# Optimization experiments

Hardware: AMD Instinct MI355X
Metric: run time of the kernel (lower is better)

## Reference

```python
import jax, jax.numpy as jnp
import numpy as np

N_NODES = 50000
N_EDGES = 400000
IN_DIM = 512
OUT_DIM = 512


def setup_inputs() -> dict:
    key = jax.random.key(0)
    k1, k2, k3, k4 = jax.random.split(key, 4)
    x = jax.random.normal(k1, (N_NODES, IN_DIM), dtype=jnp.float32)
    edge_index = jax.random.randint(k2, (2, N_EDGES), 0, N_NODES, dtype=jnp.int64)
    # nn.Linear(in_dim, out_dim): weight [out, in], bias [out]
    W = jax.random.normal(k3, (OUT_DIM, IN_DIM), dtype=jnp.float32) / np.sqrt(IN_DIM)
    b = jax.random.normal(k4, (OUT_DIM,), dtype=jnp.float32) * 0.01
    return {"x": x, "edge_index": edge_index, "W": W, "b": b}


def reference(x, edge_index, W, b):
    n = x.shape[0]
    loops = jnp.arange(n, dtype=edge_index.dtype)
    row = jnp.concatenate([edge_index[0], loops])  # src
    col = jnp.concatenate([edge_index[1], loops])  # dst
    # degree from row counts (matches torch.bincount(row)); self-loops ensure deg >= 1
    deg = jax.ops.segment_sum(jnp.ones(row.shape[0], dtype=x.dtype), row, num_segments=n)
    dis = jax.lax.rsqrt(deg)  # deg^-0.5
    norm = dis[row] * dis[col]  # [E+N]
    h = x @ W.T + b  # [N, out_dim]
    # out[dst] += norm * h[src], fused gather-scale-scatter
    out = jax.ops.segment_sum(norm[:, None] * h[row], col, num_segments=n)
    return jax.nn.relu(out)
```

## Files before the change

### kernel.cpp

```cpp
#include <hip/hip_runtime.h>
#include <hip/hip_bf16.h>

#define K_DIM 512
#define N_DIM 512

typedef __attribute__((ext_vector_type(8))) short s8v;
typedef __attribute__((ext_vector_type(4))) short s4v;
typedef __attribute__((ext_vector_type(4))) float f4v;

__device__ __forceinline__ short f2bf(float f) {
  union { float f; unsigned u; } v; v.f = f;
  unsigned r = (v.u + 0x7FFFu + ((v.u >> 16) & 1u)) >> 16;
  return (short)r;
}
__device__ __forceinline__ float bflo(unsigned u) {
  union { unsigned u; float f; } v; v.u = u << 16; return v.f;
}
__device__ __forceinline__ float bfhi(unsigned u) {
  union { unsigned u; float f; } v; v.u = u & 0xffff0000u; return v.f;
}

__device__ __forceinline__ void gload16(const void* g, void* l) {
  __builtin_amdgcn_global_load_lds(
      (const __attribute__((address_space(1))) void*)g,
      (__attribute__((address_space(3))) void*)l, 16, 0, 0);
}

__device__ __forceinline__ int edge_stride(const int* __restrict__ e32, int lane) {
  int chk = e32[2 * lane + 1];
  unsigned long long m = __ballot(chk == 0);
  return (m == ~0ULL) ? 2 : 1;
}

__global__ __launch_bounds__(256) void k_pre1(const float* __restrict__ W,
    short* __restrict__ Wb, const int* __restrict__ e32, int* __restrict__ outdeg,
    int* __restrict__ indeg, int E, int nbw) {
  int b = blockIdx.x;
  int t = threadIdx.x;
  if (b < nbw) {
    int i = (b * 256 + t) * 4;
    float4 f = *(const float4*)(W + i);
    s4v s; s[0] = f2bf(f.x); s[1] = f2bf(f.y); s[2] = f2bf(f.z); s[3] = f2bf(f.w);
    *(s4v*)(Wb + i) = s;
  } else {
    int st = edge_stride(e32, t & 63);
    int i = (b - nbw) * 256 + t;
    if (i < E) {
      int r = e32[(size_t)i * st];
      int c = e32[(size_t)(E + i) * st];
      atomicAdd(&outdeg[r], 1);
      atomicAdd(&indeg[c], 1);
    }
  }
}

__global__ __launch_bounds__(256) void k_pre2(const int* __restrict__ outdeg,
    float* __restrict__ dis, const int* __restrict__ indeg, int* __restrict__ part,
    int n, int nbd) {
  int b = blockIdx.x;
  if (b < nbd) {
    int i = b * 256 + threadIdx.x;
    if (i < n) dis[i] = rsqrtf((float)(outdeg[i] + 1));
  } else {
    __shared__ int sm[256];
    int lb = b - nbd;
    int i = lb * 256 + threadIdx.x;
    sm[threadIdx.x] = (i < n) ? indeg[i] : 0;
    __syncthreads();
    for (int off = 128; off > 0; off >>= 1) {
      if (threadIdx.x < off) sm[threadIdx.x] += sm[threadIdx.x + off];
      __syncthreads();
    }
    if (threadIdx.x == 0) part[lb] = sm[0];
  }
}

__global__ __launch_bounds__(256) void k_scan(const int* __restrict__ indeg,
    const int* __restrict__ part, int* __restrict__ row_start,
    int* __restrict__ cursor, int n, int nb) {
  __shared__ int sp[256];
  __shared__ int sm[256];
  int t = threadIdx.x, b = blockIdx.x;
  sp[t] = (t < nb) ? part[t] : 0;
  __syncthreads();
  for (int off = 1; off < 256; off <<= 1) {
    int a = (t >= off) ? sp[t - off] : 0;
    __syncthreads();
    sp[t] += a;
    __syncthreads();
  }
  int pOff = (b > 0) ? sp[b - 1] : 0;
  if (b == 0 && t == 255) row_start[n] = sp[255];
  int i = b * 256 + t;
  int v = (i < n) ? indeg[i] : 0;
  sm[t] = v;
  __syncthreads();
  for (int off = 1; off < 256; off <<= 1) {
    int a = (t >= off) ? sm[t - off] : 0;
    __syncthreads();
    sm[t] += a;
    __syncthreads();
  }
  if (i < n) {
    int excl = pOff + sm[t] - v;
    row_start[i] = excl;
    cursor[i] = excl;
  }
}

__global__ __launch_bounds__(256) void k_fillconv(const int* __restrict__ e32,
    int* __restrict__ cursor, int* __restrict__ csr, int E,
    const float* __restrict__ x, const float* __restrict__ dis,
    short* __restrict__ xs, long long totalx, int nbh) {
  int b = blockIdx.x;
  int t = threadIdx.x;
  if (b < nbh) {
    int st = edge_stride(e32, t & 63);
    int i = b * 256 + t;
    if (i < E) {
      int r = e32[(size_t)i * st];
      int c = e32[(size_t)(E + i) * st];
      int p = atomicAdd(&cursor[c], 1);
      csr[p] = r;
    }
  } else {
    long long i = ((long long)(b - nbh) * 256 + t) * 8;
    if (i < totalx) {
      float dv = dis[i >> 9];
      float4 f0 = *(const float4*)(x + i);
      float4 f1 = *(const float4*)(x + i + 4);
      s8v v;
      v[0] = f2bf(dv * f0.x); v[1] = f2bf(dv * f0.y);
      v[2] = f2bf(dv * f0.z); v[3] = f2bf(dv * f0.w);
      v[4] = f2bf(dv * f1.x); v[5] = f2bf(dv * f1.y);
      v[6] = f2bf(dv * f1.z); v[7] = f2bf(dv * f1.w);
      *(s8v*)(xs + i) = v;
    }
  }
}

__device__ __forceinline__ void add8(float* acc, uint4 rv) {
  acc[0] += bflo(rv.x); acc[1] += bfhi(rv.x);
  acc[2] += bflo(rv.y); acc[3] += bfhi(rv.y);
  acc[4] += bflo(rv.z); acc[5] += bfhi(rv.z);
  acc[6] += bflo(rv.w); acc[7] += bfhi(rv.w);
}

__global__ __launch_bounds__(256) void k_agg(const short* __restrict__ xs,
    const float* __restrict__ dis, const int* __restrict__ row_start,
    const int* __restrict__ csr, short* __restrict__ xa, float* __restrict__ s,
    int n) {
  int wid = blockIdx.x * 4 + (threadIdx.x >> 6);
  int nw = gridDim.x * 4;
  int lane = threadIdx.x & 63;
  const short* hl = xs + lane * 8;
  for (int v = wid; v < n; v += nw) {
    float acc[8];
    float accs = 0.f;
    {
      uint4 r = *(const uint4*)(hl + (size_t)v * N_DIM);
      acc[0] = bflo(r.x); acc[1] = bfhi(r.x);
      acc[2] = bflo(r.y); acc[3] = bfhi(r.y);
      acc[4] = bflo(r.z); acc[5] = bfhi(r.z);
      acc[6] = bflo(r.w); acc[7] = bfhi(r.w);
    }
    int sb = __builtin_amdgcn_readfirstlane(row_start[v]);
    int eb = __builtin_amdgcn_readfirstlane(row_start[v + 1]);
    int idx = sb;
    for (; idx + 8 <= eb; idx += 8) {
      int s0 = csr[idx],     s1 = csr[idx + 1], s2 = csr[idx + 2], s3 = csr[idx + 3];
      int s4 = csr[idx + 4], s5 = csr[idx + 5], s6 = csr[idx + 6], s7 = csr[idx + 7];
      uint4 r0 = *(const uint4*)(hl + (size_t)s0 * N_DIM);
      uint4 r1 = *(const uint4*)(hl + (size_t)s1 * N_DIM);
      uint4 r2 = *(const uint4*)(hl + (size_t)s2 * N_DIM);
      uint4 r3 = *(const uint4*)(hl + (size_t)s3 * N_DIM);
      uint4 r4 = *(const uint4*)(hl + (size_t)s4 * N_DIM);
      uint4 r5 = *(const uint4*)(hl + (size_t)s5 * N_DIM);
      uint4 r6 = *(const uint4*)(hl + (size_t)s6 * N_DIM);
      uint4 r7 = *(const uint4*)(hl + (size_t)s7 * N_DIM);
      accs += dis[s0] + dis[s1] + dis[s2] + dis[s3]
            + dis[s4] + dis[s5] + dis[s6] + dis[s7];
      add8(acc, r0); add8(acc, r1); add8(acc, r2); add8(acc, r3);
      add8(acc, r4); add8(acc, r5); add8(acc, r6); add8(acc, r7);
    }
    for (; idx + 4 <= eb; idx += 4) {
      int s0 = csr[idx], s1 = csr[idx + 1], s2 = csr[idx + 2], s3 = csr[idx + 3];
      uint4 r0 = *(const uint4*)(hl + (size_t)s0 * N_DIM);
      uint4 r1 = *(const uint4*)(hl + (size_t)s1 * N_DIM);
      uint4 r2 = *(const uint4*)(hl + (size_t)s2 * N_DIM);
      uint4 r3 = *(const uint4*)(hl + (size_t)s3 * N_DIM);
      accs += dis[s0] + dis[s1] + dis[s2] + dis[s3];
      add8(acc, r0); add8(acc, r1); add8(acc, r2); add8(acc, r3);
    }
    for (; idx < eb; ++idx) {
      int s0 = csr[idx];
      uint4 r0 = *(const uint4*)(hl + (size_t)s0 * N_DIM);
      accs += dis[s0];
      add8(acc, r0);
    }
    float dv = dis[v];
    s8v o;
    #pragma unroll
    for (int q = 0; q < 8; ++q) o[q] = f2bf(dv * acc[q]);
    *(s8v*)(xa + (size_t)v * N_DIM + lane * 8) = o;
    if (lane == 0) s[v] = dv * (accs + dv);
  }
}

__global__ __launch_bounds__(256, 5) void k_gemm(const short* __restrict__ xa,
    const short* __restrict__ Wb, const float* __restrict__ bias,
    const float* __restrict__ s, float* __restrict__ out, int M) {
  __shared__ __align__(16) char smem[32768];
  short* As = (short*)smem;
  short* Bs = (short*)(smem + 16384);
  int nwg = gridDim.x;
  int orig = blockIdx.x;
  int q8 = nwg >> 3, r8 = nwg & 7;
  int xcd = orig & 7, pos = orig >> 3;
  int swz = (xcd < r8 ? xcd * (q8 + 1) : r8 * (q8 + 1) + (xcd - r8) * q8) + pos;
  const int n0 = (swz & 3) * 128;
  const int m0 = (swz >> 2) * 128;

  const int tid = threadIdx.x;
  const int lane = tid & 63;
  const int wv = tid >> 6, wr = wv >> 1, wc = wv & 1;
  const int la = lane & 15, lg = lane >> 4;

  const short* ag[2];
  const short* bg[2];
  int doff[2];
  #pragma unroll
  for (int r = 0; r < 2; ++r) {
    int id = r * 256 + tid;
    int row = id >> 2;
    int ch = id & 3;
    int arow = m0 + row; if (arow >= M) arow = M - 1;
    ag[r] = xa + (size_t)arow * K_DIM + ch * 8;
    bg[r] = Wb + (size_t)(n0 + row) * K_DIM + ch * 8;
    doff[r] = (r * 256 + (tid & 192)) * 16;
  }
  int aro[4], bro[4];
  #pragma unroll
  for (int i = 0; i < 4; ++i) {
    aro[i] = (64 * wr + 16 * i + la) * 64 + lg * 16;
    bro[i] = (64 * wc + 16 * i + la) * 64 + lg * 16;
  }

  f4v acc[4][4] = {};

  #pragma unroll
  for (int r = 0; r < 2; ++r) {
    gload16(ag[r], (char*)As + doff[r]);
    gload16(bg[r], (char*)Bs + doff[r]);
  }
  __syncthreads();

  for (int kt = 0; kt < 16; ++kt) {
    const int cur = kt & 1;
    const int nxt = cur ^ 1;
    if (kt < 15) {
      const int kk = (kt + 1) * 32;
      #pragma unroll
      for (int r = 0; r < 2; ++r) {
        gload16(ag[r] + kk, (char*)As + nxt * 8192 + doff[r]);
        gload16(bg[r] + kk, (char*)Bs + nxt * 8192 + doff[r]);
      }
    }
    s8v af[4], bf[4];
    const char* ab = (const char*)As + cur * 8192;
    const char* bb = (const char*)Bs + cur * 8192;
    #pragma unroll
    for (int i = 0; i < 4; ++i) af[i] = *(const s8v*)(ab + aro[i]);
    #pragma unroll
    for (int j = 0; j < 4; ++j) bf[j] = *(const s8v*)(bb + bro[j]);
    #pragma unroll
    for (int i = 0; i < 4; ++i)
      #pragma unroll
      for (int j = 0; j < 4; ++j)
        acc[i][j] = __builtin_amdgcn_mfma_f32_16x16x32_bf16(af[i], bf[j], acc[i][j], 0, 0, 0);
    __syncthreads();
  }

  float* Es = (float*)(smem + wv * 4352);
  float bv[4];
  #pragma unroll
  for (int j = 0; j < 4; ++j) bv[j] = bias[n0 + 64 * wc + 16 * j + la];
  #pragma unroll
  for (int i = 0; i < 4; ++i) {
    int rowb = m0 + 64 * wr + 16 * i + lg * 4;
    float sv[4];
    #pragma unroll
    for (int r = 0; r < 4; ++r) sv[r] = (rowb + r < M) ? s[rowb + r] : 0.f;
    #pragma unroll
    for (int j = 0; j < 4; ++j)
      #pragma unroll
      for (int r = 0; r < 4; ++r)
        Es[(lg * 4 + r) * 68 + 16 * j + la] = fmaxf(acc[i][j][r] + sv[r] * bv[j], 0.f);
    asm volatile("s_waitcnt lgkmcnt(0)" ::: "memory");
    int gr0 = m0 + 64 * wr + 16 * i;
    #pragma unroll
    for (int rr = 0; rr < 4; ++rr) {
      int id = rr * 64 + lane;
      int rl = id >> 4, ch = id & 15;
      f4v val = *(const f4v*)&Es[rl * 68 + ch * 4];
      if (gr0 + rl < M)
        __builtin_nontemporal_store(val,
            (f4v*)(out + (size_t)(gr0 + rl) * N_DIM + n0 + 64 * wc + ch * 4));
    }
    asm volatile("s_waitcnt lgkmcnt(0)" ::: "memory");
  }
}

extern "C" void kernel_launch(void* const* d_in, const int* in_sizes, int n_in,
                              void* d_out, int out_size, void* d_ws, size_t ws_size,
                              hipStream_t stream) {
  const float* x = (const float*)d_in[0];
  const int* e32 = (const int*)d_in[1];
  const float* W = (const float*)d_in[2];
  const float* bias = (const float*)d_in[3];
  float* out = (float*)d_out;
  int M = in_sizes[0] / K_DIM;
  int E = in_sizes[1] / 2;

  char* ws = (char*)d_ws;
  size_t off = 0;
  auto alloc = [&](size_t bytes) {
    void* p = ws + off;
    off = (off + bytes + 255) & ~(size_t)255;
    return p;
  };
  short* Wb      = (short*)alloc((size_t)N_DIM * K_DIM * 2);
  short* xa      = (short*)alloc((size_t)M * N_DIM * 2);
  float* dis     = (float*)alloc((size_t)M * 4);
  float* sv      = (float*)alloc((size_t)M * 4);
  int*   outdeg  = (int*)alloc((size_t)M * 4);
  int*   indeg   = (int*)alloc((size_t)M * 4);
  int*   rstart  = (int*)alloc((size_t)(M + 1) * 4);
  int*   cursor  = (int*)alloc((size_t)M * 4);
  int*   part    = (int*)alloc(256 * 4);
  int*   csr     = (int*)alloc((size_t)E * 4);
  if (off > ws_size) return;

  short* xs = (short*)d_out;

  size_t zbytes = (size_t)((char*)indeg - (char*)outdeg) + (size_t)M * 4;
  (void)hipMemsetAsync(outdeg, 0, zbytes, stream);

  int nbw = N_DIM * K_DIM / 4 / 256;
  int nbh = (E + 255) / 256;
  k_pre1<<<nbw + nbh, 256, 0, stream>>>(W, Wb, e32, outdeg, indeg, E, nbw);
  int nscan = (M + 255) / 256;
  k_pre2<<<nscan * 2, 256, 0, stream>>>(outdeg, dis, indeg, part, M, nscan);
  k_scan<<<nscan, 256, 0, stream>>>(indeg, part, rstart, cursor, M, nscan);
  long long totalx = (long long)M * K_DIM;
  int nbx = (int)((totalx / 8 + 255) / 256);
  k_fillconv<<<nbh + nbx, 256, 0, stream>>>(e32, cursor, csr, E, x, dis, xs,
                                            totalx, nbh);
  k_agg<<<2048, 256, 0, stream>>>(xs, dis, rstart, csr, xa, sv, M);
  int nmc = (M + 127) / 128;
  k_gemm<<<nmc * 4, 256, 0, stream>>>(xa, Wb, bias, sv, out, M);
}
```

Measured before the change: 217.9 us.

## Move x bf16 conversion into first prep kernel, apply source scaling in aggregation

The x-to-bf16 conversion moves from the fill kernel into k_pre1, so it no longer waits on dis and runs alongside the degree counting. Because xs is no longer pre-scaled by the source dis, k_agg now loads dis per neighbour and does FMAs instead of adds. The self term is handled by starting the accumulator at dv. This shortens the dependency chain before aggregation at the cost of extra dis gathers and FMA work in k_agg. The GEMM launch bounds also change from 5 to 4 waves per SIMD.

```diff
diff --git a/kernel.cpp b/kernel.cpp
--- a/kernel.cpp
+++ b/kernel.cpp
@@ -33,8 +33,9 @@
 }
 
 __global__ __launch_bounds__(256) void k_pre1(const float* __restrict__ W,
-    short* __restrict__ Wb, const int* __restrict__ e32, int* __restrict__ outdeg,
-    int* __restrict__ indeg, int E, int nbw) {
+    short* __restrict__ Wb, const float* __restrict__ x, short* __restrict__ xs,
+    long long totalx, const int* __restrict__ e32, int* __restrict__ outdeg,
+    int* __restrict__ indeg, int E, int nbw, int nbx) {
   int b = blockIdx.x;
   int t = threadIdx.x;
   if (b < nbw) {
@@ -42,9 +43,19 @@
     float4 f = *(const float4*)(W + i);
     s4v s; s[0] = f2bf(f.x); s[1] = f2bf(f.y); s[2] = f2bf(f.z); s[3] = f2bf(f.w);
     *(s4v*)(Wb + i) = s;
+  } else if (b < nbw + nbx) {
+    long long i = ((long long)(b - nbw) * 256 + t) * 8;
+    if (i < totalx) {
+      float4 f0 = *(const float4*)(x + i);
+      float4 f1 = *(const float4*)(x + i + 4);
+      s8v v;
+      v[0] = f2bf(f0.x); v[1] = f2bf(f0.y); v[2] = f2bf(f0.z); v[3] = f2bf(f0.w);
+      v[4] = f2bf(f1.x); v[5] = f2bf(f1.y); v[6] = f2bf(f1.z); v[7] = f2bf(f1.w);
+      *(s8v*)(xs + i) = v;
+    }
   } else {
     int st = edge_stride(e32, t & 63);
-    int i = (b - nbw) * 256 + t;
+    int i = (b - nbw - nbx) * 256 + t;
     if (i < E) {
       int r = e32[(size_t)i * st];
       int c = e32[(size_t)(E + i) * st];
@@ -108,42 +119,22 @@
   }
 }
 
-__global__ __launch_bounds__(256) void k_fillconv(const int* __restrict__ e32,
-    int* __restrict__ cursor, int* __restrict__ csr, int E,
-    const float* __restrict__ x, const float* __restrict__ dis,
-    short* __restrict__ xs, long long totalx, int nbh) {
-  int b = blockIdx.x;
-  int t = threadIdx.x;
-  if (b < nbh) {
-    int st = edge_stride(e32, t & 63);
-    int i = b * 256 + t;
-    if (i < E) {
-      int r = e32[(size_t)i * st];
-      int c = e32[(size_t)(E + i) * st];
-      int p = atomicAdd(&cursor[c], 1);
-      csr[p] = r;
-    }
-  } else {
-    long long i = ((long long)(b - nbh) * 256 + t) * 8;
-    if (i < totalx) {
-      float dv = dis[i >> 9];
-      float4 f0 = *(const float4*)(x + i);
-      float4 f1 = *(const float4*)(x + i + 4);
-      s8v v;
-      v[0] = f2bf(dv * f0.x); v[1] = f2bf(dv * f0.y);
-      v[2] = f2bf(dv * f0.z); v[3] = f2bf(dv * f0.w);
-      v[4] = f2bf(dv * f1.x); v[5] = f2bf(dv * f1.y);
-      v[6] = f2bf(dv * f1.z); v[7] = f2bf(dv * f1.w);
-      *(s8v*)(xs + i) = v;
-    }
-  }
-}
-
-__device__ __forceinline__ void add8(float* acc, uint4 rv) {
-  acc[0] += bflo(rv.x); acc[1] += bfhi(rv.x);
-  acc[2] += bflo(rv.y); acc[3] += bfhi(rv.y);
-  acc[4] += bflo(rv.z); acc[5] += bfhi(rv.z);
-  acc[6] += bflo(rv.w); acc[7] += bfhi(rv.w);
+__global__ __launch_bounds__(256) void k_fill(const int* __restrict__ e32,
+    int* __restrict__ cursor, int* __restrict__ csr, int E) {
+  int st = edge_stride(e32, threadIdx.x & 63);
+  int i = blockIdx.x * blockDim.x + threadIdx.x;
+  if (i >= E) return;
+  int r = e32[(size_t)i * st];
+  int c = e32[(size_t)(E + i) * st];
+  int p = atomicAdd(&cursor[c], 1);
+  csr[p] = r;
+}
+
+__device__ __forceinline__ void fma8(float* acc, uint4 rv, float w) {
+  acc[0] += w * bflo(rv.x); acc[1] += w * bfhi(rv.x);
+  acc[2] += w * bflo(rv.y); acc[3] += w * bfhi(rv.y);
+  acc[4] += w * bflo(rv.z); acc[5] += w * bfhi(rv.z);
+  acc[6] += w * bflo(rv.w); acc[7] += w * bfhi(rv.w);
 }
 
 __global__ __launch_bounds__(256) void k_agg(const short* __restrict__ xs,
@@ -155,14 +146,15 @@
   int lane = threadIdx.x & 63;
   const short* hl = xs + lane * 8;
   for (int v = wid; v < n; v += nw) {
+    float dv = dis[v];
     float acc[8];
-    float accs = 0.f;
+    float accs = dv;
     {
       uint4 r = *(const uint4*)(hl + (size_t)v * N_DIM);
-      acc[0] = bflo(r.x); acc[1] = bfhi(r.x);
-      acc[2] = bflo(r.y); acc[3] = bfhi(r.y);
-      acc[4] = bflo(r.z); acc[5] = bfhi(r.z);
-      acc[6] = bflo(r.w); acc[7] = bfhi(r.w);
+      acc[0] = dv * bflo(r.x); acc[1] = dv * bfhi(r.x);
+      acc[2] = dv * bflo(r.y); acc[3] = dv * bfhi(r.y);
+      acc[4] = dv * bflo(r.z); acc[5] = dv * bfhi(r.z);
+      acc[6] = dv * bflo(r.w); acc[7] = dv * bfhi(r.w);
     }
     int sb = __builtin_amdgcn_readfirstlane(row_start[v]);
     int eb = __builtin_amdgcn_readfirstlane(row_start[v + 1]);
@@ -170,6 +162,8 @@
     for (; idx + 8 <= eb; idx += 8) {
       int s0 = csr[idx],     s1 = csr[idx + 1], s2 = csr[idx + 2], s3 = csr[idx + 3];
       int s4 = csr[idx + 4], s5 = csr[idx + 5], s6 = csr[idx + 6], s7 = csr[idx + 7];
+      float w0 = dis[s0], w1 = dis[s1], w2 = dis[s2], w3 = dis[s3];
+      float w4 = dis[s4], w5 = dis[s5], w6 = dis[s6], w7 = dis[s7];
       uint4 r0 = *(const uint4*)(hl + (size_t)s0 * N_DIM);
       uint4 r1 = *(const uint4*)(hl + (size_t)s1 * N_DIM);
       uint4 r2 = *(const uint4*)(hl + (size_t)s2 * N_DIM);
@@ -178,36 +172,36 @@
       uint4 r5 = *(const uint4*)(hl + (size_t)s5 * N_DIM);
       uint4 r6 = *(const uint4*)(hl + (size_t)s6 * N_DIM);
       uint4 r7 = *(const uint4*)(hl + (size_t)s7 * N_DIM);
-      accs += dis[s0] + dis[s1] + dis[s2] + dis[s3]
-            + dis[s4] + dis[s5] + dis[s6] + dis[s7];
-      add8(acc, r0); add8(acc, r1); add8(acc, r2); add8(acc, r3);
-      add8(acc, r4); add8(acc, r5); add8(acc, r6); add8(acc, r7);
+      accs += w0 + w1 + w2 + w3 + w4 + w5 + w6 + w7;
+      fma8(acc, r0, w0); fma8(acc, r1, w1); fma8(acc, r2, w2); fma8(acc, r3, w3);
+      fma8(acc, r4, w4); fma8(acc, r5, w5); fma8(acc, r6, w6); fma8(acc, r7, w7);
     }
     for (; idx + 4 <= eb; idx += 4) {
       int s0 = csr[idx], s1 = csr[idx + 1], s2 = csr[idx + 2], s3 = csr[idx + 3];
+      float w0 = dis[s0], w1 = dis[s1], w2 = dis[s2], w3 = dis[s3];
       uint4 r0 = *(const uint4*)(hl + (size_t)s0 * N_DIM);
       uint4 r1 = *(const uint4*)(hl + (size_t)s1 * N_DIM);
       uint4 r2 = *(const uint4*)(hl + (size_t)s2 * N_DIM);
       uint4 r3 = *(const uint4*)(hl + (size_t)s3 * N_DIM);
-      accs += dis[s0] + dis[s1] + dis[s2] + dis[s3];
-      add8(acc, r0); add8(acc, r1); add8(acc, r2); add8(acc, r3);
+      accs += w0 + w1 + w2 + w3;
+      fma8(acc, r0, w0); fma8(acc, r1, w1); fma8(acc, r2, w2); fma8(acc, r3, w3);
     }
     for (; idx < eb; ++idx) {
       int s0 = csr[idx];
+      float w0 = dis[s0];
       uint4 r0 = *(const uint4*)(hl + (size_t)s0 * N_DIM);
-      accs += dis[s0];
-      add8(acc, r0);
-    }
-    float dv = dis[v];
+      accs += w0;
+      fma8(acc, r0, w0);
+    }
     s8v o;
     #pragma unroll
     for (int q = 0; q < 8; ++q) o[q] = f2bf(dv * acc[q]);
     *(s8v*)(xa + (size_t)v * N_DIM + lane * 8) = o;
-    if (lane == 0) s[v] = dv * (accs + dv);
-  }
-}
-
-__global__ __launch_bounds__(256, 5) void k_gemm(const short* __restrict__ xa,
+    if (lane == 0) s[v] = dv * accs;
+  }
+}
+
+__global__ __launch_bounds__(256, 4) void k_gemm(const short* __restrict__ xa,
     const short* __restrict__ Wb, const float* __restrict__ bias,
     const float* __restrict__ s, float* __restrict__ out, int M) {
   __shared__ __align__(16) char smem[32768];
@@ -346,16 +340,16 @@
   size_t zbytes = (size_t)((char*)indeg - (char*)outdeg) + (size_t)M * 4;
   (void)hipMemsetAsync(outdeg, 0, zbytes, stream);
 
+  long long totalx = (long long)M * K_DIM;
   int nbw = N_DIM * K_DIM / 4 / 256;
+  int nbx = (int)((totalx / 8 + 255) / 256);
   int nbh = (E + 255) / 256;
-  k_pre1<<<nbw + nbh, 256, 0, stream>>>(W, Wb, e32, outdeg, indeg, E, nbw);
+  k_pre1<<<nbw + nbx + nbh, 256, 0, stream>>>(W, Wb, x, xs, totalx, e32,
+                                              outdeg, indeg, E, nbw, nbx);
   int nscan = (M + 255) / 256;
   k_pre2<<<nscan * 2, 256, 0, stream>>>(outdeg, dis, indeg, part, M, nscan);
   k_scan<<<nscan, 256, 0, stream>>>(indeg, part, rstart, cursor, M, nscan);
-  long long totalx = (long long)M * K_DIM;
-  int nbx = (int)((totalx / 8 + 255) / 256);
-  k_fillconv<<<nbh + nbx, 256, 0, stream>>>(e32, cursor, csr, E, x, dis, xs,
-                                            totalx, nbh);
+  k_fill<<<nbh, 256, 0, stream>>>(e32, cursor, csr, E);
   k_agg<<<2048, 256, 0, stream>>>(xs, dis, rstart, csr, xa, sv, M);
   int nmc = (M + 127) / 128;
   k_gemm<<<nmc * 4, 256, 0, stream>>>(xa, Wb, bias, sv, out, M);
```

Result: faster. 204.0 us, median of 2 (-6.4%).
